# Kernel tuning notes

Hardware: AMD Instinct MI355X
Metric: run time of the kernel (lower is better)

## Reference

```python
import jax, jax.numpy as jnp
import numpy as np

N1, D1 = 16, 64
IN_SPECS = [(512, 8), (512, 8)]  # (num_in_caps, dim_in_caps) per input layer
TOTAL_IN = sum(n for n, _ in IN_SPECS)
B = 16
EPS = 1e-5


def _kaiming_normal(key, shape):
    # kaiming_normal_(mode='fan_in', nonlinearity='relu'): std = sqrt(2/fan_in)
    # For a 4D tensor [N1, num_in, dim_in, D1], torch fan_in = dim_in * D1
    fan_in = shape[2] * shape[3]
    std = np.sqrt(2.0 / fan_in)
    return jax.random.normal(key, shape, dtype=jnp.float32) * std


def setup_inputs() -> dict:
    key = jax.random.key(0)
    ks = jax.random.split(key, 2 + len(IN_SPECS))
    x0 = jax.random.normal(ks[0], (B, IN_SPECS[0][0], IN_SPECS[0][1]), dtype=jnp.float32)
    x1 = jax.random.normal(ks[1], (B, IN_SPECS[1][0], IN_SPECS[1][1]), dtype=jnp.float32)
    W0 = _kaiming_normal(ks[2], (N1, IN_SPECS[0][0], IN_SPECS[0][1], D1))
    W1 = _kaiming_normal(ks[3], (N1, IN_SPECS[1][0], IN_SPECS[1][1], D1))
    b = jnp.zeros((N1, TOTAL_IN, TOTAL_IN), dtype=jnp.float32)
    return {"x0": x0, "x1": x1, "W0": W0, "W1": W1, "b": b}


def _squash(x):
    sq = jnp.sum(x * x, axis=-1, keepdims=True)  # squared norm
    return (sq / (1.0 + sq)) * x / (jnp.sqrt(sq) + EPS)


def reference(x0, x1, W0, W1, b):
    # Per-input capsule projections: [B,i,j] x [k,i,j,l] -> [B,k,i,l]
    U0 = jnp.einsum('bij,kijl->bkil', x0, W0)
    U1 = jnp.einsum('bij,kijl->bkil', x1, W1)
    U = jnp.concatenate([U0, U1], axis=2)  # [B, N1, TOTAL_IN, D1]
    scale = jnp.sqrt(jnp.asarray(D1, dtype=jnp.float32))
    # Attention-like agreement matrix: [B, N1, TOTAL_IN, TOTAL_IN]
    A = jnp.einsum('bkil,bkzl->bkiz', U, U) / scale
    C = jax.nn.softmax(A, axis=-1) + b  # post-softmax learned additive bias
    # S[b,k,l] = sum_i sum_z U[b,k,i,l] * C[b,k,i,z]  (contracts both i and z)
    S = jnp.einsum('bkil,bki->bkl', U, jnp.sum(C, axis=-1))  # [B, N1, D1]
    return _squash(S)
```

## Files before the change

### kernel.cpp

```cpp
#include <hip/hip_runtime.h>


__global__ __launch_bounds__(256) void proj_kernel(
        const float* __restrict__ x0, const float* __restrict__ x1,
        const float* __restrict__ W0, const float* __restrict__ W1,
        const float* __restrict__ bias, float* __restrict__ partial) {
    __shared__ float xs[16 * 132];
    __shared__ float ssum[16];
    __shared__ float rbuf[4 * 8 * 64];
    const int tid = threadIdx.x;
    const int k     = blockIdx.x >> 6;
    const int chunk = blockIdx.x & 63;
    const int g  = tid >> 4;
    const int q  = tid & 15;
    const int w  = tid >> 6;
    const int gw = g & 3;

    const int layer = chunk >> 5;
    const int i0    = (chunk & 31) * 16;
    const int ig0   = chunk * 16;
    const float* __restrict__ x = layer ? x1 : x0;
    const float* __restrict__ W = layer ? W1 : W0;

    const float4* Wf4 = (const float4*)W;
    const size_t wbase = (size_t)(k * 512 + i0 + g) * 128 + q;
    float4 wv[8];
#pragma unroll
    for (int j = 0; j < 8; ++j) wv[j] = Wf4[wbase + j * 16];

    const float4* xp = (const float4*)(x + (size_t)(g * 512 + i0 + q) * 8);
    float4 a0 = xp[0], a1 = xp[1];

    {
        const float4* bp = (const float4*)(bias + (size_t)(k * 1024 + ig0 + g) * 1024);
        float s0 = 0.f, s1 = 0.f, s2 = 0.f, s3 = 0.f;
#pragma unroll
        for (int batch = 0; batch < 2; ++batch) {
            float4 v[8];
#pragma unroll
            for (int it = 0; it < 8; ++it) v[it] = bp[q + 16 * (batch * 8 + it)];
#pragma unroll
            for (int it = 0; it < 8; it += 4) {
                s0 += v[it].x + v[it].y + v[it].z + v[it].w;
                s1 += v[it + 1].x + v[it + 1].y + v[it + 1].z + v[it + 1].w;
                s2 += v[it + 2].x + v[it + 2].y + v[it + 2].z + v[it + 2].w;
                s3 += v[it + 3].x + v[it + 3].y + v[it + 3].z + v[it + 3].w;
            }
        }
        float s = (s0 + s1) + (s2 + s3);
#pragma unroll
        for (int m = 8; m >= 1; m >>= 1) s += __shfl_xor(s, m);
        if (q == 0) ssum[g] = 1.0f + s;
    }
    __syncthreads();

    {
        const float s = ssum[q];
        float4* dst = (float4*)&xs[q * 132 + g * 8];
        dst[0] = make_float4(a0.x * s, a0.y * s, a0.z * s, a0.w * s);
        dst[1] = make_float4(a1.x * s, a1.y * s, a1.z * s, a1.w * s);
    }
    __syncthreads();

#pragma unroll
    for (int half = 0; half < 2; ++half) {
        float4 acc[8];
#pragma unroll
        for (int bi = 0; bi < 8; ++bi) acc[bi] = make_float4(0.f, 0.f, 0.f, 0.f);
#pragma unroll
        for (int bi = 0; bi < 8; ++bi) {
            const int b = half * 8 + bi;
            float xr[8];
            *(float4*)&xr[0] = *(const float4*)&xs[g * 132 + b * 8];
            *(float4*)&xr[4] = *(const float4*)&xs[g * 132 + b * 8 + 4];
#pragma unroll
            for (int j = 0; j < 8; ++j) {
                acc[bi].x += xr[j] * wv[j].x;
                acc[bi].y += xr[j] * wv[j].y;
                acc[bi].z += xr[j] * wv[j].z;
                acc[bi].w += xr[j] * wv[j].w;
            }
        }
#pragma unroll
        for (int bi = 0; bi < 8; ++bi) {
            acc[bi].x += __shfl_xor(acc[bi].x, 32); acc[bi].x += __shfl_xor(acc[bi].x, 16);
            acc[bi].y += __shfl_xor(acc[bi].y, 32); acc[bi].y += __shfl_xor(acc[bi].y, 16);
            acc[bi].z += __shfl_xor(acc[bi].z, 32); acc[bi].z += __shfl_xor(acc[bi].z, 16);
            acc[bi].w += __shfl_xor(acc[bi].w, 32); acc[bi].w += __shfl_xor(acc[bi].w, 16);
        }
        if (gw == 0) {
#pragma unroll
            for (int bi = 0; bi < 8; ++bi)
                *(float4*)&rbuf[(w * 8 + bi) * 64 + q * 4] = acc[bi];
        }
        __syncthreads();
        {
            const int bi = tid >> 5;
            const int l  = tid & 31;
            float v0 = 0.f, v1 = 0.f;
#pragma unroll
            for (int ww = 0; ww < 4; ++ww) {
                v0 += rbuf[(ww * 8 + bi) * 64 + l];
                v1 += rbuf[(ww * 8 + bi) * 64 + l + 32];
            }
            const int b = half * 8 + bi;
            partial[(size_t)blockIdx.x * 1024 + b * 64 + l]      = v0;
            partial[(size_t)blockIdx.x * 1024 + b * 64 + l + 32] = v1;
        }
        __syncthreads();
    }
}

__global__ __launch_bounds__(256) void reduce_squash_kernel(
        const float* __restrict__ partial, float* __restrict__ out) {
    __shared__ float red[4][64];
    const int row = blockIdx.x;
    const int b = row >> 4, k = row & 15;
    const int w = threadIdx.x >> 6, lane = threadIdx.x & 63;
    float s = 0.f;
#pragma unroll
    for (int cc = 0; cc < 16; ++cc) {
        const int c = w + cc * 4;
        s += partial[((size_t)(k * 64 + c)) * 1024 + b * 64 + lane];
    }
    red[w][lane] = s;
    __syncthreads();
    if (w == 0) {
        float v = red[0][lane] + red[1][lane] + red[2][lane] + red[3][lane];
        float sq = v * v;
#pragma unroll
        for (int m = 32; m >= 1; m >>= 1) sq += __shfl_xor(sq, m);
        out[(size_t)row * 64 + lane] = (sq / (1.0f + sq)) * v / (sqrtf(sq) + 1e-5f);
    }
}

extern "C" void kernel_launch(void* const* d_in, const int* in_sizes, int n_in,
                              void* d_out, int out_size, void* d_ws, size_t ws_size,
                              hipStream_t stream) {
    const float* x0  = (const float*)d_in[0];
    const float* x1  = (const float*)d_in[1];
    const float* W0  = (const float*)d_in[2];
    const float* W1  = (const float*)d_in[3];
    const float* bia = (const float*)d_in[4];
    float* out = (float*)d_out;

    float* partial = (float*)d_ws;

    proj_kernel<<<dim3(1024), dim3(256), 0, stream>>>(x0, x1, W0, W1, bia, partial);
    reduce_squash_kernel<<<dim3(256), dim3(256), 0, stream>>>(partial, out);
}
```

Before: 27.77 us.

## Split capsule chunks in half and double projection grid to 2048 blocks

```diff
diff --git a/kernel.cpp b/kernel.cpp
--- a/kernel.cpp
+++ b/kernel.cpp
@@ -5,60 +5,57 @@
         const float* __restrict__ x0, const float* __restrict__ x1,
         const float* __restrict__ W0, const float* __restrict__ W1,
         const float* __restrict__ bias, float* __restrict__ partial) {
-    __shared__ float xs[16 * 132];
-    __shared__ float ssum[16];
+    __shared__ float xs[8 * 132];
+    __shared__ float ssum[8];
     __shared__ float rbuf[4 * 8 * 64];
     const int tid = threadIdx.x;
-    const int k     = blockIdx.x >> 6;
-    const int chunk = blockIdx.x & 63;
-    const int g  = tid >> 4;
-    const int q  = tid & 15;
+    const int k     = blockIdx.x >> 7;
+    const int chunk = blockIdx.x & 127;
+    const int g  = tid >> 5;
+    const int h  = tid & 31;
+    const int jb = (tid >> 4) & 1;
+    const int lq = tid & 15;
     const int w  = tid >> 6;
-    const int gw = g & 3;
 
-    const int layer = chunk >> 5;
-    const int i0    = (chunk & 31) * 16;
-    const int ig0   = chunk * 16;
+    const int layer = chunk >> 6;
+    const int i0    = (chunk & 63) * 8;
+    const int ig0   = chunk * 8;
     const float* __restrict__ x = layer ? x1 : x0;
     const float* __restrict__ W = layer ? W1 : W0;
 
     const float4* Wf4 = (const float4*)W;
-    const size_t wbase = (size_t)(k * 512 + i0 + g) * 128 + q;
-    float4 wv[8];
+    const size_t wbase = (size_t)(k * 512 + i0 + g) * 128 + jb * 64 + lq;
+    float4 wv[4];
 #pragma unroll
-    for (int j = 0; j < 8; ++j) wv[j] = Wf4[wbase + j * 16];
+    for (int j4 = 0; j4 < 4; ++j4) wv[j4] = Wf4[wbase + j4 * 16];
 
-    const float4* xp = (const float4*)(x + (size_t)(g * 512 + i0 + q) * 8);
-    float4 a0 = xp[0], a1 = xp[1];
+    const int xb = tid >> 4, xrl = (tid >> 1) & 7, xh = tid & 1;
+    const float4 a = ((const float4*)(x + (size_t)(xb * 512 + i0 + xrl) * 8))[xh];
 
     {
         const float4* bp = (const float4*)(bias + (size_t)(k * 1024 + ig0 + g) * 1024);
+        float4 v[8];
+#pragma unroll
+        for (int it = 0; it < 8; ++it) v[it] = bp[h + 32 * it];
         float s0 = 0.f, s1 = 0.f, s2 = 0.f, s3 = 0.f;
 #pragma unroll
-        for (int batch = 0; batch < 2; ++batch) {
-            float4 v[8];
-#pragma unroll
-            for (int it = 0; it < 8; ++it) v[it] = bp[q + 16 * (batch * 8 + it)];
-#pragma unroll
-            for (int it = 0; it < 8; it += 4) {
-                s0 += v[it].x + v[it].y + v[it].z + v[it].w;
-                s1 += v[it + 1].x + v[it + 1].y + v[it + 1].z + v[it + 1].w;
-                s2 += v[it + 2].x + v[it + 2].y + v[it + 2].z + v[it + 2].w;
-                s3 += v[it + 3].x + v[it + 3].y + v[it + 3].z + v[it + 3].w;
-            }
+        for (int it = 0; it < 8; it += 4) {
+            s0 += v[it].x + v[it].y + v[it].z + v[it].w;
+            s1 += v[it + 1].x + v[it + 1].y + v[it + 1].z + v[it + 1].w;
+            s2 += v[it + 2].x + v[it + 2].y + v[it + 2].z + v[it + 2].w;
+            s3 += v[it + 3].x + v[it + 3].y + v[it + 3].z + v[it + 3].w;
         }
         float s = (s0 + s1) + (s2 + s3);
 #pragma unroll
-        for (int m = 8; m >= 1; m >>= 1) s += __shfl_xor(s, m);
-        if (q == 0) ssum[g] = 1.0f + s;
+        for (int m = 16; m >= 1; m >>= 1) s += __shfl_xor(s, m);
+        if (h == 0) ssum[g] = 1.0f + s;
     }
     __syncthreads();
 
     {
-        const float s = ssum[q];
-        float4* dst = (float4*)&xs[q * 132 + g * 8];
-        dst[0] = make_float4(a0.x * s, a0.y * s, a0.z * s, a0.w * s);
-        dst[1] = make_float4(a1.x * s, a1.y * s, a1.z * s, a1.w * s);
+        const float s = ssum[xrl];
+        *(float4*)&xs[xrl * 132 + xb * 8 + xh * 4] =
+            make_float4(a.x * s, a.y * s, a.z * s, a.w * s);
     }
     __syncthreads();
 
@@ -70,28 +67,23 @@
 #pragma unroll
         for (int bi = 0; bi < 8; ++bi) {
             const int b = half * 8 + bi;
-            float xr[8];
-            *(float4*)&xr[0] = *(const float4*)&xs[g * 132 + b * 8];
-            *(float4*)&xr[4] = *(const float4*)&xs[g * 132 + b * 8 + 4];
-#pragma unroll
-            for (int j = 0; j < 8; ++j) {
-                acc[bi].x += xr[j] * wv[j].x;
-                acc[bi].y += xr[j] * wv[j].y;
-                acc[bi].z += xr[j] * wv[j].z;
-                acc[bi].w += xr[j] * wv[j].w;
-            }
+            const float4 xv = *(const float4*)&xs[g * 132 + b * 8 + jb * 4];
+            acc[bi].x += xv.x * wv[0].x + xv.y * wv[1].x + xv.z * wv[2].x + xv.w * wv[3].x;
+            acc[bi].y += xv.x * wv[0].y + xv.y * wv[1].y + xv.z * wv[2].y + xv.w * wv[3].y;
+            acc[bi].z += xv.x * wv[0].z + xv.y * wv[1].z + xv.z * wv[2].z + xv.w * wv[3].z;
+            acc[bi].w += xv.x * wv[0].w + xv.y * wv[1].w + xv.z * wv[2].w + xv.w * wv[3].w;
         }
 #pragma unroll
         for (int bi = 0; bi < 8; ++bi) {
-            acc[bi].x += __shfl_xor(acc[bi].x, 32); acc[bi].x += __shfl_xor(acc[bi].x, 16);
-            acc[bi].y += __shfl_xor(acc[bi].y, 32); acc[bi].y += __shfl_xor(acc[bi].y, 16);
-            acc[bi].z += __shfl_xor(acc[bi].z, 32); acc[bi].z += __shfl_xor(acc[bi].z, 16);
-            acc[bi].w += __shfl_xor(acc[bi].w, 32); acc[bi].w += __shfl_xor(acc[bi].w, 16);
+            acc[bi].x += __shfl_xor(acc[bi].x, 16); acc[bi].x += __shfl_xor(acc[bi].x, 32);
+            acc[bi].y += __shfl_xor(acc[bi].y, 16); acc[bi].y += __shfl_xor(acc[bi].y, 32);
+            acc[bi].z += __shfl_xor(acc[bi].z, 16); acc[bi].z += __shfl_xor(acc[bi].z, 32);
+            acc[bi].w += __shfl_xor(acc[bi].w, 16); acc[bi].w += __shfl_xor(acc[bi].w, 32);
         }
-        if (gw == 0) {
+        if ((tid & 48) == 0) {
 #pragma unroll
             for (int bi = 0; bi < 8; ++bi)
-                *(float4*)&rbuf[(w * 8 + bi) * 64 + q * 4] = acc[bi];
+                *(float4*)&rbuf[(w * 8 + bi) * 64 + lq * 4] = acc[bi];
         }
         __syncthreads();
         {
@@ -119,9 +111,9 @@
     const int w = threadIdx.x >> 6, lane = threadIdx.x & 63;
     float s = 0.f;
 #pragma unroll
-    for (int cc = 0; cc < 16; ++cc) {
+    for (int cc = 0; cc < 32; ++cc) {
         const int c = w + cc * 4;
-        s += partial[((size_t)(k * 64 + c)) * 1024 + b * 64 + lane];
+        s += partial[((size_t)(k * 128 + c)) * 1024 + b * 64 + lane];
     }
     red[w][lane] = s;
     __syncthreads();
@@ -146,6 +138,6 @@
 
     float* partial = (float*)d_ws;
 
-    proj_kernel<<<dim3(1024), dim3(256), 0, stream>>>(x0, x1, W0, W1, bia, partial);
+    proj_kernel<<<dim3(2048), dim3(256), 0, stream>>>(x0, x1, W0, W1, bia, partial);
     reduce_squash_kernel<<<dim3(256), dim3(256), 0, stream>>>(partial, out);
 }
```

Result: slower. 30.95 us (+11.5%).

## Overlap bias row-sum loads with projection FMAs by applying scale after accumulation

Applied to the files above, without the earlier changes.

```diff
diff --git a/kernel.cpp b/kernel.cpp
--- a/kernel.cpp
+++ b/kernel.cpp
@@ -6,7 +6,6 @@
         const float* __restrict__ W0, const float* __restrict__ W1,
         const float* __restrict__ bias, float* __restrict__ partial) {
     __shared__ float xs[16 * 132];
-    __shared__ float ssum[16];
     __shared__ float rbuf[4 * 8 * 64];
     const int tid = threadIdx.x;
     const int k     = blockIdx.x >> 6;
@@ -22,45 +21,27 @@
     const float* __restrict__ x = layer ? x1 : x0;
     const float* __restrict__ W = layer ? W1 : W0;
 
+    const float4* xp = (const float4*)(x + (size_t)(g * 512 + i0 + q) * 8);
+    float4 a0 = xp[0], a1 = xp[1];
+
     const float4* Wf4 = (const float4*)W;
     const size_t wbase = (size_t)(k * 512 + i0 + g) * 128 + q;
     float4 wv[8];
 #pragma unroll
     for (int j = 0; j < 8; ++j) wv[j] = Wf4[wbase + j * 16];
 
-    const float4* xp = (const float4*)(x + (size_t)(g * 512 + i0 + q) * 8);
-    float4 a0 = xp[0], a1 = xp[1];
+    const float4* bp = (const float4*)(bias + (size_t)(k * 1024 + ig0 + g) * 1024);
+    float4 va[8];
+#pragma unroll
+    for (int it = 0; it < 8; ++it) va[it] = bp[q + 16 * it];
 
-    {
-        const float4* bp = (const float4*)(bias + (size_t)(k * 1024 + ig0 + g) * 1024);
-        float s0 = 0.f, s1 = 0.f, s2 = 0.f, s3 = 0.f;
-#pragma unroll
-        for (int batch = 0; batch < 2; ++batch) {
-            float4 v[8];
-#pragma unroll
-            for (int it = 0; it < 8; ++it) v[it] = bp[q + 16 * (batch * 8 + it)];
-#pragma unroll
-            for (int it = 0; it < 8; it += 4) {
-                s0 += v[it].x + v[it].y + v[it].z + v[it].w;
-                s1 += v[it + 1].x + v[it + 1].y + v[it + 1].z + v[it + 1].w;
-                s2 += v[it + 2].x + v[it + 2].y + v[it + 2].z + v[it + 2].w;
-                s3 += v[it + 3].x + v[it + 3].y + v[it + 3].z + v[it + 3].w;
-            }
-        }
-        float s = (s0 + s1) + (s2 + s3);
-#pragma unroll
-        for (int m = 8; m >= 1; m >>= 1) s += __shfl_xor(s, m);
-        if (q == 0) ssum[g] = 1.0f + s;
-    }
-    __syncthreads();
+    *(float4*)&xs[q * 132 + g * 8]     = a0;
+    *(float4*)&xs[q * 132 + g * 8 + 4] = a1;
+    asm volatile("s_waitcnt lgkmcnt(0)" ::: "memory");
+    __builtin_amdgcn_s_barrier();
+    __builtin_amdgcn_sched_barrier(0);
 
-    {
-        const float s = ssum[q];
-        float4* dst = (float4*)&xs[q * 132 + g * 8];
-        dst[0] = make_float4(a0.x * s, a0.y * s, a0.z * s, a0.w * s);
-        dst[1] = make_float4(a1.x * s, a1.y * s, a1.z * s, a1.w * s);
-    }
-    __syncthreads();
+    float scale = 0.f;
 
 #pragma unroll
     for (int half = 0; half < 2; ++half) {
@@ -81,6 +62,38 @@
                 acc[bi].w += xr[j] * wv[j].w;
             }
         }
+
+        if (half == 0) {
+            float s0 = 0.f, s1 = 0.f, s2 = 0.f, s3 = 0.f;
+#pragma unroll
+            for (int it = 0; it < 8; it += 4) {
+                s0 += va[it].x + va[it].y + va[it].z + va[it].w;
+                s1 += va[it + 1].x + va[it + 1].y + va[it + 1].z + va[it + 1].w;
+                s2 += va[it + 2].x + va[it + 2].y + va[it + 2].z + va[it + 2].w;
+                s3 += va[it + 3].x + va[it + 3].y + va[it + 3].z + va[it + 3].w;
+            }
+            float4 vb[8];
+#pragma unroll
+            for (int it = 0; it < 8; ++it) vb[it] = bp[q + 16 * (8 + it)];
+#pragma unroll
+            for (int it = 0; it < 8; it += 4) {
+                s0 += vb[it].x + vb[it].y + vb[it].z + vb[it].w;
+                s1 += vb[it + 1].x + vb[it + 1].y + vb[it + 1].z + vb[it + 1].w;
+                s2 += vb[it + 2].x + vb[it + 2].y + vb[it + 2].z + vb[it + 2].w;
+                s3 += vb[it + 3].x + vb[it + 3].y + vb[it + 3].z + vb[it + 3].w;
+            }
+            float s = (s0 + s1) + (s2 + s3);
+#pragma unroll
+            for (int m = 8; m >= 1; m >>= 1) s += __shfl_xor(s, m);
+            scale = 1.0f + s;
+        }
+
+#pragma unroll
+        for (int bi = 0; bi < 8; ++bi) {
+            acc[bi].x *= scale; acc[bi].y *= scale;
+            acc[bi].z *= scale; acc[bi].w *= scale;
+        }
+
 #pragma unroll
         for (int bi = 0; bi < 8; ++bi) {
             acc[bi].x += __shfl_xor(acc[bi].x, 32); acc[bi].x += __shfl_xor(acc[bi].x, 16);
```

After: 30.33 us. 9.2% more time.
